# Kernel tuning notes

Measured on AMD Instinct MI355X. Metric: run time of the kernel, lower is better.

The kernel has to match this reference:

```python
import jax, jax.numpy as jnp
import numpy as np

_EPSILON = 1e-06


def _allocation(usage):
    """Freeness-based allocation: sort usage, exclusive cumprod, scatter back.

    usage: [B, M] in [0, 1]. Returns allocation weights [B, M].
    """
    usage = _EPSILON + (1.0 - _EPSILON) * usage
    nonusage = 1.0 - usage
    m = usage.shape[-1]
    sorted_nonusage, indices = jax.lax.top_k(nonusage, k=m)  # descending nonusage = ascending usage
    sorted_usage = 1.0 - sorted_nonusage
    # exclusive cumulative product along the sorted memory axis
    prod_sorted_usage = jnp.concatenate(
        [jnp.ones_like(sorted_usage[:, :1]),
         jnp.cumprod(sorted_usage, axis=1)[:, :-1]], axis=1)
    sorted_allocation = sorted_nonusage * prod_sorted_usage
    # invert the permutation and gather back to original slot order
    inverse_indices = jnp.argsort(indices, axis=1)
    return jnp.take_along_axis(sorted_allocation, inverse_indices, axis=1)


def _updated_usage(write_weights, free_gate, read_weights, prev_usage):
    """Freeness.__call__: usage after write then after read/free. [B, M]."""
    ww = jax.lax.stop_gradient(write_weights)
    # usage after write: increase toward 1 at written slots
    write_w = 1.0 - jnp.prod(1.0 - ww, axis=1)          # [B, M]
    usage = prev_usage + (1.0 - prev_usage) * write_w
    # usage after read: decrease where free_gate*read_weights is high
    free_read = free_gate[:, :, None] * read_weights      # [B, R, M]
    phi = jnp.prod(1.0 - free_read, axis=1)               # [B, M]
    return usage * phi


def _write_allocation_weights(usage, write_gates, num_writes):
    """Per-write-head allocation weights. Returns [B, num_writes, M]."""
    wg = write_gates[:, :, None]                          # [B, W, 1]
    allocs = []
    for i in range(num_writes):  # small fixed head count; sequential by construction
        a = _allocation(usage)
        allocs.append(a)
        usage = usage + (1.0 - usage) * wg[:, i, :] * a
    return jnp.stack(allocs, axis=1)


def setup_inputs() -> dict:
    key = jax.random.key(0)
    ks = jax.random.split(key, 5)
    B, W, R, M = 512, 4, 8, 16384
    return {
        "write_weights": jax.random.uniform(ks[0], (B, W, M), dtype=jnp.float32),
        "free_gate": jax.random.uniform(ks[1], (B, R), dtype=jnp.float32),
        "read_weights": jax.random.uniform(ks[2], (B, R, M), dtype=jnp.float32),
        "prev_usage": jax.random.uniform(ks[3], (B, M), dtype=jnp.float32),
        "write_gates": jax.random.uniform(ks[4], (B, W), dtype=jnp.float32),
        "num_writes": W,
    }


def reference(write_weights, free_gate, read_weights, prev_usage, write_gates, num_writes):
    usage = _updated_usage(write_weights, free_gate, read_weights, prev_usage)
    alloc = _write_allocation_weights(usage, write_gates, num_writes)
    return usage, alloc
```

## Files before the change

kernel.cpp:

```cpp
#include <hip/hip_runtime.h>
#include <stdint.h>

typedef unsigned long long u64;
typedef unsigned int u32;
typedef float f32x4 __attribute__((ext_vector_type(4)));

#define NBINS 512
#define CAP 512
#define LOG_CUT (-64.0f)
#define NT 1024

__device__ __forceinline__ int bucket_of(u32 nnbits) {
    u32 d = 0x3F800000u - nnbits;
    if (d == 0u) d = 1u;
    const int e = 31 - __builtin_clz(d);
    const u32 sub = (e >= 4) ? ((d >> (e - 4)) & 15u) : ((d << (4 - e)) & 15u);
    int v = (e << 4) | (int)sub;
    if (v > NBINS - 1) v = NBINS - 1;
    return (NBINS - 1) - v;
}

__device__ __forceinline__ void nt_store4(float* p, float4 v) {
    f32x4 nv;
    nv.x = v.x; nv.y = v.y; nv.z = v.z; nv.w = v.w;
    __builtin_nontemporal_store(nv, (f32x4*)p);
}

template <int TW, int TR>
__global__ __launch_bounds__(NT, 8)
void fused_kernel(const float* __restrict__ ww,
                  const float* __restrict__ fg,
                  const float* __restrict__ rw,
                  const float* __restrict__ prev,
                  const float* __restrict__ wgt,
                  float* __restrict__ out_usage,
                  float* __restrict__ out_alloc,
                  int B, int W, int R, int M)
{
    __shared__ u64   keyS[CAP];
    __shared__ float logS[CAP];
    __shared__ u32   hC[NBINS];
    __shared__ float mB[NBINS];
    __shared__ u32   tc[16];
    __shared__ float twv[16];
    __shared__ int   misc[4];
    extern __shared__ float uS[];

    const int Wl = TW > 0 ? TW : W;
    const int Rl = TR > 0 ? TR : R;
    const int b = blockIdx.x;
    const int t = threadIdx.x;
    const int lane = t & 63;
    const int wid = t >> 6;

    const float C1 = (float)(1.0 - 1e-6);
    const float CE = 1e-6f;

    if (t < NBINS) {
        hC[t] = 0u;
        const int v = NBINS - 1 - t;
        const int e = v >> 4;
        const u32 sub = (u32)(v & 15);
        const int sh = e >= 4 ? e - 4 : 0;
        u64 dhi64 = ((u64)(17u + sub) << sh) + 1u;
        u32 dhi = dhi64 > 0x3F800000ull ? 0x3F800000u : (u32)dhi64;
        const float nnlo = __uint_as_float(0x3F800000u - dhi);
        float ueub = 1.0f - nnlo;
        ueub = ueub < 1e-38f ? 1e-38f : (ueub > 0.9999999f ? 0.9999999f : ueub);
        mB[t] = __log2f(ueub);
    }
    __syncthreads();

    {
        const size_t rowOff = (size_t)b * M;
        float frs[TR > 0 ? TR : 8];
        #pragma unroll
        for (int r = 0; r < Rl; ++r) frs[r] = fg[(size_t)b * Rl + r];

        const float4 z = make_float4(0.f, 0.f, 0.f, 0.f);
        for (int m = t * 4; m < M; m += NT * 4) {
            const float4 pv = *(const float4*)(prev + rowOff + m);
            float pr0 = 1.f, pr1 = 1.f, pr2 = 1.f, pr3 = 1.f;
            #pragma unroll
            for (int w = 0; w < Wl; ++w) {
                const float4 a = *(const float4*)(ww + ((size_t)b * Wl + w) * M + m);
                pr0 *= (1.0f - a.x); pr1 *= (1.0f - a.y);
                pr2 *= (1.0f - a.z); pr3 *= (1.0f - a.w);
            }
            float u0 = pv.x + (1.0f - pv.x) * (1.0f - pr0);
            float u1 = pv.y + (1.0f - pv.y) * (1.0f - pr1);
            float u2 = pv.z + (1.0f - pv.z) * (1.0f - pr2);
            float u3 = pv.w + (1.0f - pv.w) * (1.0f - pr3);
            float f0 = 1.f, f1 = 1.f, f2 = 1.f, f3 = 1.f;
            #pragma unroll
            for (int r = 0; r < Rl; ++r) {
                const float fr = frs[r];
                const float4 a = *(const float4*)(rw + ((size_t)b * Rl + r) * M + m);
                f0 *= (1.0f - fr * a.x); f1 *= (1.0f - fr * a.y);
                f2 *= (1.0f - fr * a.z); f3 *= (1.0f - fr * a.w);
            }
            float4 uo;
            uo.x = u0 * f0; uo.y = u1 * f1; uo.z = u2 * f2; uo.w = u3 * f3;
            *(float4*)(uS + m) = uo;
            nt_store4(out_usage + rowOff + m, uo);
            #pragma unroll
            for (int w = 0; w < Wl; ++w)
                nt_store4(out_alloc + ((size_t)b * Wl + w) * M + m, z);
            const float ua[4] = {uo.x, uo.y, uo.z, uo.w};
            #pragma unroll
            for (int j = 0; j < 4; ++j) {
                const float nn = 1.0f - (CE + C1 * ua[j]);
                atomicAdd(&hC[bucket_of(__float_as_uint(nn))], 1u);
            }
        }
    }

    for (int i = 0; i < Wl; ++i) {
        const float wgi = wgt[(size_t)b * Wl + i];
        float* orow = out_alloc + ((size_t)b * Wl + i) * M;

        if (t == 0) { misc[0] = 0; misc[1] = -1; misc[2] = NBINS; }
        __syncthreads();

        {
            const bool act = (t < NBINS);
            u32 sc = 0; float sw = 0.f; int x = 0;
            if (act) {
                x = NBINS - 1 - t;
                const u32 c = hC[x];
                sc = c;
                sw = mB[x] * (float)c;
                #pragma unroll
                for (int off = 1; off < 64; off <<= 1) {
                    const u32  oc = __shfl_up(sc, off);
                    const float ow = __shfl_up(sw, off);
                    if (lane >= off) { sc += oc; sw += ow; }
                }
                if (lane == 63) { tc[wid] = sc; twv[wid] = sw; }
            }
            __syncthreads();
            if (act) {
                u32 ac = 0; float aw = 0.f;
                for (int q = 0; q < wid; ++q) { ac += tc[q]; aw += twv[q]; }
                sc += ac; sw += aw;
                if (sw <= LOG_CUT) atomicMax(&misc[1], x);
                if (sc <= (u32)CAP) atomicMin(&misc[2], x);
            }
        }
        __syncthreads();
        const int xs = misc[1];
        const int xc = misc[2];
        const int cut = (xs > xc) ? xs : xc;

        for (int x = t; x < M; x += NT) {
            const float u = uS[x];
            const float ue = CE + C1 * u;
            const float nn = 1.0f - ue;
            const int bkt = bucket_of(__float_as_uint(nn));
            const bool pred = (bkt >= cut) && (cut < NBINS);
            const u64 mask = __ballot(pred);
            const int cnt = __popcll(mask);
            if (cnt) {
                int base = 0;
                if (lane == 0) base = atomicAdd(&misc[0], cnt);
                base = __shfl(base, 0);
                if (pred) {
                    const int pos = base + __popcll(mask & ((1ull << lane) - 1));
                    if (pos < CAP) {
                        keyS[pos] = (((u64)(~__float_as_uint(nn))) << 14) | (u64)(u32)x;
                        logS[pos] = __log2f(ue);
                    }
                }
            }
        }
        __syncthreads();
        int K = misc[0]; if (K > CAP) K = CAP;

        if (t < K) {
            const u64 mykey = keyS[t];
            float S = 0.0f;
            #pragma unroll 4
            for (int k = 0; k < K; ++k) {
                const u64 kk = keyS[k];
                const float lg = logS[k];
                if (kk < mykey) S += lg;
            }
            const u32 nnbits = ~((u32)(mykey >> 14));
            const float nn = __uint_as_float(nnbits);
            const int idx = (int)(mykey & 0x3FFFull);
            const float al = nn * __builtin_exp2f(S);
            if (al != 0.0f) {
                orow[idx] = al;
                if (i + 1 < Wl) {
                    const float u0v = uS[idx];
                    const float unew = u0v + ((1.0f - u0v) * wgi) * al;
                    uS[idx] = unew;
                    const int bold = bucket_of(nnbits);
                    const float nn2 = 1.0f - (CE + C1 * unew);
                    const int bnew = bucket_of(__float_as_uint(nn2));
                    if (bnew != bold) {
                        atomicSub(&hC[bold], 1u);
                        atomicAdd(&hC[bnew], 1u);
                    }
                }
            }
        }
        __syncthreads();
    }
}

extern "C" void kernel_launch(void* const* d_in, const int* in_sizes, int n_in,
                              void* d_out, int out_size, void* d_ws, size_t ws_size,
                              hipStream_t stream) {
    const float* ww   = (const float*)d_in[0];
    const float* fg   = (const float*)d_in[1];
    const float* rw   = (const float*)d_in[2];
    const float* prev = (const float*)d_in[3];
    const float* wgt  = (const float*)d_in[4];
    const int BWM = in_sizes[0];
    const int BR  = in_sizes[1];
    const int BM  = in_sizes[3];
    const int BW  = in_sizes[4];
    const int M = BWM / BW;
    const int B = BM / M;
    const int W = BW / B;
    const int R = BR / B;

    float* out_usage = (float*)d_out;
    float* out_alloc = out_usage + (size_t)BM;

    const size_t smem = (size_t)M * sizeof(float);
    if (W == 4 && R == 8) {
        hipLaunchKernelGGL((fused_kernel<4, 8>), dim3(B), dim3(NT), smem, stream,
                           ww, fg, rw, prev, wgt, out_usage, out_alloc, B, W, R, M);
    } else {
        hipLaunchKernelGGL((fused_kernel<0, 0>), dim3(B), dim3(NT), smem, stream,
                           ww, fg, rw, prev, wgt, out_usage, out_alloc, B, W, R, M);
    }
}
```

Measured before the change: 149.0 us.

## Replace full-row LDS usage buffer with compact candidate pool across write heads

Drops the 64KB dynamic shared-memory copy of the usage row. Instead it builds, once, a pool of up to 2048 lowest-usage slots read back from the global usage output, and each write head rescans only that pool rather than all M slots. Pool entries are updated in place after each head's allocation. The goal is lower LDS footprint, which allows more blocks per CU, and less per-head scan work. The cost is an extra global re-read of usage and a 16-bit index packing, and it assumes the pool covers every slot that later heads allocate to.

Result: no change. 146.4 us (-1.7%).

```diff
diff --git a/kernel.cpp b/kernel.cpp
--- a/kernel.cpp
+++ b/kernel.cpp
@@ -3,10 +3,12 @@
 
 typedef unsigned long long u64;
 typedef unsigned int u32;
+typedef unsigned short u16;
 typedef float f32x4 __attribute__((ext_vector_type(4)));
 
 #define NBINS 512
-#define CAP 512
+#define CAP 256
+#define POOLCAP 2048
 #define LOG_CUT (-64.0f)
 #define NT 1024
 
@@ -37,14 +39,16 @@
                   float* __restrict__ out_alloc,
                   int B, int W, int R, int M)
 {
-    __shared__ u64   keyS[CAP];
-    __shared__ float logS[CAP];
+    __shared__ u64   poolKey[POOLCAP];
+    __shared__ float poolLg[POOLCAP];
+    __shared__ u64   candKey[CAP];
+    __shared__ float candLg[CAP];
+    __shared__ u16   candPos[CAP];
     __shared__ u32   hC[NBINS];
     __shared__ float mB[NBINS];
     __shared__ u32   tc[16];
     __shared__ float twv[16];
-    __shared__ int   misc[4];
-    extern __shared__ float uS[];
+    __shared__ int   misc[6];
 
     const int Wl = TW > 0 ? TW : W;
     const int Rl = TR > 0 ? TR : R;
@@ -55,6 +59,7 @@
 
     const float C1 = (float)(1.0 - 1e-6);
     const float CE = 1e-6f;
+    const size_t rowOff = (size_t)b * M;
 
     if (t < NBINS) {
         hC[t] = 0u;
@@ -69,10 +74,10 @@
         ueub = ueub < 1e-38f ? 1e-38f : (ueub > 0.9999999f ? 0.9999999f : ueub);
         mB[t] = __log2f(ueub);
     }
+    if (t == 0) { misc[0] = 0; misc[3] = NBINS; }
     __syncthreads();
 
     {
-        const size_t rowOff = (size_t)b * M;
         float frs[TR > 0 ? TR : 8];
         #pragma unroll
         for (int r = 0; r < Rl; ++r) frs[r] = fg[(size_t)b * Rl + r];
@@ -101,8 +106,7 @@
             }
             float4 uo;
             uo.x = u0 * f0; uo.y = u1 * f1; uo.z = u2 * f2; uo.w = u3 * f3;
-            *(float4*)(uS + m) = uo;
-            nt_store4(out_usage + rowOff + m, uo);
+            *(float4*)(out_usage + rowOff + m) = uo;
             #pragma unroll
             for (int w = 0; w < Wl; ++w)
                 nt_store4(out_alloc + ((size_t)b * Wl + w) * M + m, z);
@@ -114,12 +118,66 @@
             }
         }
     }
+    __syncthreads();
+
+    {
+        const bool act = (t < NBINS);
+        u32 sc = 0; int x = 0;
+        if (act) {
+            x = NBINS - 1 - t;
+            sc = hC[x];
+            #pragma unroll
+            for (int off = 1; off < 64; off <<= 1) {
+                const u32 oc = __shfl_up(sc, off);
+                if (lane >= off) sc += oc;
+            }
+            if (lane == 63) tc[wid] = sc;
+        }
+        __syncthreads();
+        if (act) {
+            u32 ac = 0;
+            for (int q = 0; q < wid; ++q) ac += tc[q];
+            sc += ac;
+            if (sc <= (u32)POOLCAP) atomicMin(&misc[3], x);
+        }
+    }
+    __syncthreads();
+    const int pc = misc[3];
+
+    for (int m = t * 4; m < M; m += NT * 4) {
+        const float4 uu = *(const float4*)(out_usage + rowOff + m);
+        const float ua[4] = {uu.x, uu.y, uu.z, uu.w};
+        #pragma unroll
+        for (int j = 0; j < 4; ++j) {
+            const float ue = CE + C1 * ua[j];
+            const float nn = 1.0f - ue;
+            const u32 nnbits = __float_as_uint(nn);
+            const int bkt = bucket_of(nnbits);
+            const bool pred = (bkt >= pc) && (pc < NBINS);
+            const u64 mask = __ballot(pred);
+            const int cnt = __popcll(mask);
+            if (cnt) {
+                int base = 0;
+                if (lane == 0) base = atomicAdd(&misc[0], cnt);
+                base = __shfl(base, 0);
+                if (pred) {
+                    const int pos = base + __popcll(mask & ((1ull << lane) - 1));
+                    if (pos < POOLCAP) {
+                        poolKey[pos] = (((u64)(~nnbits)) << 16) | (u64)(u32)(m + j);
+                        poolLg[pos] = __log2f(ue);
+                    }
+                }
+            }
+        }
+    }
+    __syncthreads();
+    int P = misc[0]; if (P > POOLCAP) P = POOLCAP;
 
     for (int i = 0; i < Wl; ++i) {
         const float wgi = wgt[(size_t)b * Wl + i];
         float* orow = out_alloc + ((size_t)b * Wl + i) * M;
 
-        if (t == 0) { misc[0] = 0; misc[1] = -1; misc[2] = NBINS; }
+        if (t == 0) { misc[4] = 0; misc[1] = -1; misc[2] = NBINS; }
         __syncthreads();
 
         {
@@ -143,8 +201,10 @@
                 u32 ac = 0; float aw = 0.f;
                 for (int q = 0; q < wid; ++q) { ac += tc[q]; aw += twv[q]; }
                 sc += ac; sw += aw;
-                if (sw <= LOG_CUT) atomicMax(&misc[1], x);
-                if (sc <= (u32)CAP) atomicMin(&misc[2], x);
+                if (x >= pc) {
+                    if (sw <= LOG_CUT) atomicMax(&misc[1], x);
+                    if (sc <= (u32)CAP) atomicMin(&misc[2], x);
+                }
             }
         }
         __syncthreads();
@@ -152,52 +212,56 @@
         const int xc = misc[2];
         const int cut = (xs > xc) ? xs : xc;
 
-        for (int x = t; x < M; x += NT) {
-            const float u = uS[x];
-            const float ue = CE + C1 * u;
-            const float nn = 1.0f - ue;
-            const int bkt = bucket_of(__float_as_uint(nn));
+        for (int p = t; p < P; p += NT) {
+            const u64 key = poolKey[p];
+            const u32 nnbits = ~((u32)(key >> 16));
+            const int bkt = bucket_of(nnbits);
             const bool pred = (bkt >= cut) && (cut < NBINS);
             const u64 mask = __ballot(pred);
             const int cnt = __popcll(mask);
             if (cnt) {
                 int base = 0;
-                if (lane == 0) base = atomicAdd(&misc[0], cnt);
+                if (lane == 0) base = atomicAdd(&misc[4], cnt);
                 base = __shfl(base, 0);
                 if (pred) {
                     const int pos = base + __popcll(mask & ((1ull << lane) - 1));
                     if (pos < CAP) {
-                        keyS[pos] = (((u64)(~__float_as_uint(nn))) << 14) | (u64)(u32)x;
-                        logS[pos] = __log2f(ue);
+                        candKey[pos] = key;
+                        candLg[pos] = poolLg[p];
+                        candPos[pos] = (u16)p;
                     }
                 }
             }
         }
         __syncthreads();
-        int K = misc[0]; if (K > CAP) K = CAP;
+        int K = misc[4]; if (K > CAP) K = CAP;
 
         if (t < K) {
-            const u64 mykey = keyS[t];
+            const u64 mykey = candKey[t];
             float S = 0.0f;
             #pragma unroll 4
             for (int k = 0; k < K; ++k) {
-                const u64 kk = keyS[k];
-                const float lg = logS[k];
+                const u64 kk = candKey[k];
+                const float lg = candLg[k];
                 if (kk < mykey) S += lg;
             }
-            const u32 nnbits = ~((u32)(mykey >> 14));
+            const u32 nnbits = ~((u32)(mykey >> 16));
             const float nn = __uint_as_float(nnbits);
-            const int idx = (int)(mykey & 0x3FFFull);
+            const int idx = (int)(mykey & 0xFFFFull);
             const float al = nn * __builtin_exp2f(S);
             if (al != 0.0f) {
                 orow[idx] = al;
                 if (i + 1 < Wl) {
-                    const float u0v = uS[idx];
-                    const float unew = u0v + ((1.0f - u0v) * wgi) * al;
-                    uS[idx] = unew;
+                    const float u0v = 1.0f - (nn + CE) / C1;
+                    const float ucur = (1.0f - nn - CE) / C1;
+                    const float unew = ucur + ((1.0f - ucur) * wgi) * al;
+                    const float nn2 = 1.0f - (CE + C1 * unew);
+                    const u32 nn2bits = __float_as_uint(nn2);
+                    const int p = (int)candPos[t];
+                    poolKey[p] = (((u64)(~nn2bits)) << 16) | (u64)(u32)idx;
+                    poolLg[p] = __log2f(1.0f - nn2);
                     const int bold = bucket_of(nnbits);
-                    const float nn2 = 1.0f - (CE + C1 * unew);
-                    const int bnew = bucket_of(__float_as_uint(nn2));
+                    const int bnew = bucket_of(nn2bits);
                     if (bnew != bold) {
                         atomicSub(&hC[bold], 1u);
                         atomicAdd(&hC[bnew], 1u);
@@ -229,12 +293,11 @@
     float* out_usage = (float*)d_out;
     float* out_alloc = out_usage + (size_t)BM;
 
-    const size_t smem = (size_t)M * sizeof(float);
     if (W == 4 && R == 8) {
-        hipLaunchKernelGGL((fused_kernel<4, 8>), dim3(B), dim3(NT), smem, stream,
+        hipLaunchKernelGGL((fused_kernel<4, 8>), dim3(B), dim3(NT), 0, stream,
                            ww, fg, rw, prev, wgt, out_usage, out_alloc, B, W, R, M);
     } else {
-        hipLaunchKernelGGL((fused_kernel<0, 0>), dim3(B), dim3(NT), smem, stream,
+        hipLaunchKernelGGL((fused_kernel<0, 0>), dim3(B), dim3(NT), 0, stream,
                            ww, fg, rw, prev, wgt, out_usage, out_alloc, B, W, R, M);
     }
 }
```
